# Optimization experiments

Measured on AMD Instinct MI355X. Metric: run time of the kernel, lower is better.

The kernel has to match this reference:

```python
import jax, jax.numpy as jnp
import numpy as np

_W = jnp.array([10., 9., 8., 7., 6., 5., 4., 3., 2., 1.], dtype=jnp.float32)
_W_NORM = _W / jnp.sum(_W)  # np.average normalizes by weight sum (55)


def setup_inputs() -> dict:
    key = jax.random.key(0)
    k1, k2 = jax.random.split(key)
    x = jax.random.randint(k1, (1024, 64, 10), 0, 8000, dtype=jnp.int32)
    table = jax.random.normal(k2, (8000, 256), dtype=jnp.float32)
    return {"x": x, "table": table}


def reference(x, table):
    # Gather per-char vectors: [T, F, 10, D]
    vecs = table[x]
    # Weighted average over the 10 chars (weights [10..1], normalized)
    return jnp.einsum('tfcd,c->tfd', vecs, _W_NORM)
```

## Files before the change

### kernel.cpp

```cpp
#include <hip/hip_runtime.h>
#include <hip/hip_bf16.h>


#define ROWS_TOTAL (1024 * 64)

typedef float v4f __attribute__((ext_vector_type(4)));

__global__ __launch_bounds__(256)
void char2vec_sliced2(const int* __restrict__ x,
                      const float* __restrict__ table,
                      float* __restrict__ out) {
    const int slice = blockIdx.x & 7;
    const int rgrp  = blockIdx.x >> 3;
    const int wave  = threadIdx.x >> 6;
    const int lane  = threadIdx.x & 63;

    const int row0 = rgrp * 64 + wave * 16 + (lane >> 3) * 2;
    const int row1 = row0 + 1;
    const int d    = slice * 32 + (lane & 7) * 4;

    const int2* __restrict__ xa = reinterpret_cast<const int2*>(x + row0 * 10);
    const int2* __restrict__ xb = reinterpret_cast<const int2*>(x + row1 * 10);
    int2 pa[5], pb[5];
#pragma unroll
    for (int i = 0; i < 5; ++i) pa[i] = xa[i];
#pragma unroll
    for (int i = 0; i < 5; ++i) pb[i] = xb[i];

    int ia[10], ib[10];
#pragma unroll
    for (int i = 0; i < 5; ++i) {
        ia[2 * i] = pa[i].x; ia[2 * i + 1] = pa[i].y;
        ib[2 * i] = pb[i].x; ib[2 * i + 1] = pb[i].y;
    }

    v4f va[10], vb[10];
#pragma unroll
    for (int c = 0; c < 10; ++c)
        va[c] = *reinterpret_cast<const v4f*>(table + (size_t)ia[c] * 256 + d);
#pragma unroll
    for (int c = 0; c < 10; ++c)
        vb[c] = *reinterpret_cast<const v4f*>(table + (size_t)ib[c] * 256 + d);

    const float w[10] = {10.f / 55.f, 9.f / 55.f, 8.f / 55.f, 7.f / 55.f,
                         6.f / 55.f,  5.f / 55.f, 4.f / 55.f, 3.f / 55.f,
                         2.f / 55.f,  1.f / 55.f};

    v4f acc0 = (v4f)0.0f, acc1 = (v4f)0.0f;
#pragma unroll
    for (int c = 0; c < 10; ++c) {
        acc0 += va[c] * w[c];
        acc1 += vb[c] * w[c];
    }

    __builtin_nontemporal_store(
        acc0, reinterpret_cast<v4f*>(out + (size_t)row0 * 256 + d));
    __builtin_nontemporal_store(
        acc1, reinterpret_cast<v4f*>(out + (size_t)row1 * 256 + d));
}

extern "C" void kernel_launch(void* const* d_in, const int* in_sizes, int n_in,
                              void* d_out, int out_size, void* d_ws, size_t ws_size,
                              hipStream_t stream) {
    const int*   x     = (const int*)d_in[0];
    const float* table = (const float*)d_in[1];
    float*       out   = (float*)d_out;

    const int blocks = (ROWS_TOTAL / 64) * 8;
    char2vec_sliced2<<<blocks, 256, 0, stream>>>(x, table, out);
}
```

Baseline: 31.95 us.

## Gather from fp16 copy of embedding table with wider per-thread tiles

Adds a pre-pass kernel that converts the fp32 table to fp16 in workspace on every call. The main kernel then gathers 16-byte fp16 vectors of 8 elements and accumulates in fp32, and each block now covers 128 rows. The aim is to halve gather traffic and raise bytes per load, at the cost of an extra conversion launch, a full pass over the table, and fp16 rounding error on the table values.

```diff
diff --git a/kernel.cpp b/kernel.cpp
--- a/kernel.cpp
+++ b/kernel.cpp
@@ -1,10 +1,85 @@
 #include <hip/hip_runtime.h>
-#include <hip/hip_bf16.h>
+#include <hip/hip_fp16.h>
 
 
-#define ROWS_TOTAL (1024 * 64)
+#define ROWS_TOTAL  (1024 * 64)
+#define TABLE_ROWS  8000
+#define TABLE_D     256
 
 typedef float v4f __attribute__((ext_vector_type(4)));
+typedef _Float16 h8 __attribute__((ext_vector_type(8)));
+
+__global__ __launch_bounds__(256)
+void cvt_table_f16(const float* __restrict__ t, _Float16* __restrict__ o) {
+    const size_t i = (size_t)blockIdx.x * 256 + threadIdx.x;
+    v4f v = *reinterpret_cast<const v4f*>(t + i * 4);
+    _Float16 r[4];
+    r[0] = (_Float16)v.x; r[1] = (_Float16)v.y;
+    r[2] = (_Float16)v.z; r[3] = (_Float16)v.w;
+    *reinterpret_cast<ushort4*>(o + i * 4) = *reinterpret_cast<ushort4*>(r);
+}
+
+__global__ __launch_bounds__(256)
+void char2vec_f16w(const int* __restrict__ x,
+                   const _Float16* __restrict__ tb,
+                   float* __restrict__ out) {
+    const int slice = blockIdx.x & 7;
+    const int rgrp  = blockIdx.x >> 3;
+    const int wave  = threadIdx.x >> 6;
+    const int lane  = threadIdx.x & 63;
+    const int g     = lane >> 2;
+    const int li    = lane & 3;
+
+    const int row0 = rgrp * 128 + wave * 32 + g * 2;
+    const int row1 = row0 + 1;
+    const int d    = slice * 32 + li * 8;
+
+    const int4* __restrict__ xi = reinterpret_cast<const int4*>(x + row0 * 10);
+    int4 q0 = xi[0], q1 = xi[1], q2 = xi[2], q3 = xi[3], q4 = xi[4];
+
+    int ia[10], ib[10];
+    ia[0] = q0.x; ia[1] = q0.y; ia[2] = q0.z; ia[3] = q0.w;
+    ia[4] = q1.x; ia[5] = q1.y; ia[6] = q1.z; ia[7] = q1.w;
+    ia[8] = q2.x; ia[9] = q2.y;
+    ib[0] = q2.z; ib[1] = q2.w;
+    ib[2] = q3.x; ib[3] = q3.y; ib[4] = q3.z; ib[5] = q3.w;
+    ib[6] = q4.x; ib[7] = q4.y; ib[8] = q4.z; ib[9] = q4.w;
+
+    h8 va[10], vb[10];
+#pragma unroll
+    for (int c = 0; c < 10; ++c)
+        va[c] = *reinterpret_cast<const h8*>(tb + (size_t)ia[c] * TABLE_D + d);
+#pragma unroll
+    for (int c = 0; c < 10; ++c)
+        vb[c] = *reinterpret_cast<const h8*>(tb + (size_t)ib[c] * TABLE_D + d);
+
+    const float w[10] = {10.f / 55.f, 9.f / 55.f, 8.f / 55.f, 7.f / 55.f,
+                         6.f / 55.f,  5.f / 55.f, 4.f / 55.f, 3.f / 55.f,
+                         2.f / 55.f,  1.f / 55.f};
+
+    float a0[8] = {0, 0, 0, 0, 0, 0, 0, 0};
+    float a1[8] = {0, 0, 0, 0, 0, 0, 0, 0};
+#pragma unroll
+    for (int c = 0; c < 10; ++c) {
+#pragma unroll
+        for (int e = 0; e < 8; ++e) {
+            a0[e] = fmaf((float)va[c][e], w[c], a0[e]);
+            a1[e] = fmaf((float)vb[c][e], w[c], a1[e]);
+        }
+    }
+
+    v4f s0lo = {a0[0], a0[1], a0[2], a0[3]};
+    v4f s0hi = {a0[4], a0[5], a0[6], a0[7]};
+    v4f s1lo = {a1[0], a1[1], a1[2], a1[3]};
+    v4f s1hi = {a1[4], a1[5], a1[6], a1[7]};
+
+    float* o0 = out + (size_t)row0 * 256 + d;
+    float* o1 = out + (size_t)row1 * 256 + d;
+    __builtin_nontemporal_store(s0lo, reinterpret_cast<v4f*>(o0));
+    __builtin_nontemporal_store(s0hi, reinterpret_cast<v4f*>(o0 + 4));
+    __builtin_nontemporal_store(s1lo, reinterpret_cast<v4f*>(o1));
+    __builtin_nontemporal_store(s1hi, reinterpret_cast<v4f*>(o1 + 4));
+}
 
 __global__ __launch_bounds__(256)
 void char2vec_sliced2(const int* __restrict__ x,
@@ -37,10 +112,10 @@
     v4f va[10], vb[10];
 #pragma unroll
     for (int c = 0; c < 10; ++c)
-        va[c] = *reinterpret_cast<const v4f*>(table + (size_t)ia[c] * 256 + d);
+        va[c] = *reinterpret_cast<const v4f*>(table + (size_t)ia[c] * TABLE_D + d);
 #pragma unroll
     for (int c = 0; c < 10; ++c)
-        vb[c] = *reinterpret_cast<const v4f*>(table + (size_t)ib[c] * 256 + d);
+        vb[c] = *reinterpret_cast<const v4f*>(table + (size_t)ib[c] * TABLE_D + d);
 
     const float w[10] = {10.f / 55.f, 9.f / 55.f, 8.f / 55.f, 7.f / 55.f,
                          6.f / 55.f,  5.f / 55.f, 4.f / 55.f, 3.f / 55.f,
@@ -66,6 +141,16 @@
     const float* table = (const float*)d_in[1];
     float*       out   = (float*)d_out;
 
-    const int blocks = (ROWS_TOTAL / 64) * 8;
-    char2vec_sliced2<<<blocks, 256, 0, stream>>>(x, table, out);
+    const size_t f16_bytes = (size_t)TABLE_ROWS * TABLE_D * sizeof(_Float16);
+
+    if (ws_size >= f16_bytes) {
+        _Float16* tb = (_Float16*)d_ws;
+        const int cvt_blocks = (TABLE_ROWS * TABLE_D / 4) / 256;
+        cvt_table_f16<<<cvt_blocks, 256, 0, stream>>>(table, tb);
+        const int blocks = (ROWS_TOTAL / 128) * 8;
+        char2vec_f16w<<<blocks, 256, 0, stream>>>(x, tb, out);
+    } else {
+        const int blocks = (ROWS_TOTAL / 64) * 8;
+        char2vec_sliced2<<<blocks, 256, 0, stream>>>(x, table, out);
+    }
 }
```

After: 40.32 us. 26.2% more time.

## Convert embedding table to fp16 in workspace and gather half-precision rows

Applied to the files above, without the earlier changes.

Adds a pre-pass that converts the fp32 table to fp16 in the workspace buffer, then gathers fp16 rows with one wave per output row and accumulates in fp32. The aim is to halve the bytes read by the random gathers, at the cost of an extra launch that reads 8 MB and writes 4 MB each call. Rounding the table to fp16 loses precision, which may exceed tolerance. The original fp32 kernel remains as a fallback when the workspace is too small.

```diff
diff --git a/kernel.cpp b/kernel.cpp
--- a/kernel.cpp
+++ b/kernel.cpp
@@ -1,10 +1,59 @@
 #include <hip/hip_runtime.h>
-#include <hip/hip_bf16.h>
+#include <hip/hip_fp16.h>
 
 
-#define ROWS_TOTAL (1024 * 64)
+#define ROWS_TOTAL  (1024 * 64)
+#define TABLE_ROWS  8000
+#define TABLE_D     256
 
 typedef float v4f __attribute__((ext_vector_type(4)));
+typedef _Float16 h4 __attribute__((ext_vector_type(4)));
+
+__global__ __launch_bounds__(256)
+void cvt_table_f16(const float* __restrict__ t, _Float16* __restrict__ o) {
+    const size_t i = (size_t)blockIdx.x * 256 + threadIdx.x;
+    v4f v = *reinterpret_cast<const v4f*>(t + i * 4);
+    _Float16 r[4];
+    r[0] = (_Float16)v.x; r[1] = (_Float16)v.y;
+    r[2] = (_Float16)v.z; r[3] = (_Float16)v.w;
+    *reinterpret_cast<ushort4*>(o + i * 4) = *reinterpret_cast<ushort4*>(r);
+}
+
+__global__ __launch_bounds__(256)
+void char2vec_row(const int* __restrict__ x,
+                  const _Float16* __restrict__ tb,
+                  float* __restrict__ out) {
+    const int wave = threadIdx.x >> 6;
+    const int lane = threadIdx.x & 63;
+    const int row  = blockIdx.x * 4 + wave;
+    const int d    = lane * 4;
+
+    const int2* __restrict__ xi = reinterpret_cast<const int2*>(x + row * 10);
+    int2 p0 = xi[0], p1 = xi[1], p2 = xi[2], p3 = xi[3], p4 = xi[4];
+    int idx[10] = {p0.x, p0.y, p1.x, p1.y, p2.x,
+                   p2.y, p3.x, p3.y, p4.x, p4.y};
+
+    h4 v[10];
+#pragma unroll
+    for (int c = 0; c < 10; ++c)
+        v[c] = *reinterpret_cast<const h4*>(tb + (size_t)idx[c] * TABLE_D + d);
+
+    const float w[10] = {10.f / 55.f, 9.f / 55.f, 8.f / 55.f, 7.f / 55.f,
+                         6.f / 55.f,  5.f / 55.f, 4.f / 55.f, 3.f / 55.f,
+                         2.f / 55.f,  1.f / 55.f};
+
+    v4f acc = (v4f)0.0f;
+#pragma unroll
+    for (int c = 0; c < 10; ++c) {
+        acc.x = fmaf((float)v[c][0], w[c], acc.x);
+        acc.y = fmaf((float)v[c][1], w[c], acc.y);
+        acc.z = fmaf((float)v[c][2], w[c], acc.z);
+        acc.w = fmaf((float)v[c][3], w[c], acc.w);
+    }
+
+    __builtin_nontemporal_store(
+        acc, reinterpret_cast<v4f*>(out + (size_t)row * 256 + d));
+}
 
 __global__ __launch_bounds__(256)
 void char2vec_sliced2(const int* __restrict__ x,
@@ -37,10 +86,10 @@
     v4f va[10], vb[10];
 #pragma unroll
     for (int c = 0; c < 10; ++c)
-        va[c] = *reinterpret_cast<const v4f*>(table + (size_t)ia[c] * 256 + d);
+        va[c] = *reinterpret_cast<const v4f*>(table + (size_t)ia[c] * TABLE_D + d);
 #pragma unroll
     for (int c = 0; c < 10; ++c)
-        vb[c] = *reinterpret_cast<const v4f*>(table + (size_t)ib[c] * 256 + d);
+        vb[c] = *reinterpret_cast<const v4f*>(table + (size_t)ib[c] * TABLE_D + d);
 
     const float w[10] = {10.f / 55.f, 9.f / 55.f, 8.f / 55.f, 7.f / 55.f,
                          6.f / 55.f,  5.f / 55.f, 4.f / 55.f, 3.f / 55.f,
@@ -66,6 +115,16 @@
     const float* table = (const float*)d_in[1];
     float*       out   = (float*)d_out;
 
-    const int blocks = (ROWS_TOTAL / 64) * 8;
-    char2vec_sliced2<<<blocks, 256, 0, stream>>>(x, table, out);
+    const size_t f16_bytes = (size_t)TABLE_ROWS * TABLE_D * sizeof(_Float16);
+
+    if (ws_size >= f16_bytes) {
+        _Float16* tb = (_Float16*)d_ws;
+        const int cvt_blocks = (TABLE_ROWS * TABLE_D / 4) / 256;
+        cvt_table_f16<<<cvt_blocks, 256, 0, stream>>>(table, tb);
+        const int blocks = ROWS_TOTAL / 4;
+        char2vec_row<<<blocks, 256, 0, stream>>>(x, tb, out);
+    } else {
+        const int blocks = (ROWS_TOTAL / 64) * 8;
+        char2vec_sliced2<<<blocks, 256, 0, stream>>>(x, table, out);
+    }
 }
```

After: 40.00 us. 25.2% more time.

## Convert table to permuted fp16 in workspace and gather half-width rows

Applied to the files above, without the earlier changes.

Adds a pre-pass kernel that converts the fp32 embedding table to fp16 in the workspace, permuted so each lane reads eight halves covering two four-float output chunks. The main kernel then gathers 16-byte fp16 vectors, accumulates in fp32, and has each wave handle two full rows, with indices loaded once and shared via shuffles. This halves the gather bytes but adds a full-table conversion launch on every call and loses precision relative to fp32 inputs.

```diff
diff --git a/kernel.cpp b/kernel.cpp
--- a/kernel.cpp
+++ b/kernel.cpp
@@ -1,10 +1,70 @@
 #include <hip/hip_runtime.h>
-#include <hip/hip_bf16.h>
+#include <hip/hip_fp16.h>
 
 
 #define ROWS_TOTAL (1024 * 64)
+#define TROWS 8000
+#define TD 256
 
 typedef float v4f __attribute__((ext_vector_type(4)));
+typedef _Float16 h8 __attribute__((ext_vector_type(8)));
+
+__global__ __launch_bounds__(256)
+void cvt_perm(const float* __restrict__ t, _Float16* __restrict__ o) {
+    const int tid = blockIdx.x * 256 + threadIdx.x;
+    const int row = tid >> 5;
+    const int m   = tid & 31;
+    const float* src = t + (size_t)row * TD + 4 * m;
+    v4f a = *reinterpret_cast<const v4f*>(src);
+    v4f b = *reinterpret_cast<const v4f*>(src + 128);
+    h8 r;
+    r[0] = (_Float16)a.x; r[1] = (_Float16)a.y;
+    r[2] = (_Float16)a.z; r[3] = (_Float16)a.w;
+    r[4] = (_Float16)b.x; r[5] = (_Float16)b.y;
+    r[6] = (_Float16)b.z; r[7] = (_Float16)b.w;
+    __builtin_nontemporal_store(r, reinterpret_cast<h8*>(o + (size_t)tid * 8));
+}
+
+__global__ __launch_bounds__(256)
+void char2vec_hw(const int* __restrict__ x,
+                 const _Float16* __restrict__ tb,
+                 float* __restrict__ out) {
+    const int l    = threadIdx.x & 63;
+    const int wave = threadIdx.x >> 6;
+    const int row0 = (blockIdx.x * 4 + wave) * 2;
+    const int half = l >> 5;
+    const int m    = l & 31;
+    const int row  = row0 + half;
+
+    const int t = x[row0 * 10 + (l < 20 ? l : 19)];
+
+    int idx[10];
+#pragma unroll
+    for (int c = 0; c < 10; ++c) idx[c] = __shfl(t, half * 10 + c);
+
+    h8 v[10];
+#pragma unroll
+    for (int c = 0; c < 10; ++c)
+        v[c] = *reinterpret_cast<const h8*>(tb + (size_t)idx[c] * TD + m * 8);
+
+    const float w[10] = {10.f / 55.f, 9.f / 55.f, 8.f / 55.f, 7.f / 55.f,
+                         6.f / 55.f,  5.f / 55.f, 4.f / 55.f, 3.f / 55.f,
+                         2.f / 55.f,  1.f / 55.f};
+
+    float acc[8] = {0, 0, 0, 0, 0, 0, 0, 0};
+#pragma unroll
+    for (int c = 0; c < 10; ++c) {
+#pragma unroll
+        for (int e = 0; e < 8; ++e)
+            acc[e] = fmaf((float)v[c][e], w[c], acc[e]);
+    }
+
+    v4f lo = {acc[0], acc[1], acc[2], acc[3]};
+    v4f hi = {acc[4], acc[5], acc[6], acc[7]};
+    float* orow = out + (size_t)row * TD;
+    __builtin_nontemporal_store(lo, reinterpret_cast<v4f*>(orow + 4 * m));
+    __builtin_nontemporal_store(hi, reinterpret_cast<v4f*>(orow + 128 + 4 * m));
+}
 
 __global__ __launch_bounds__(256)
 void char2vec_sliced2(const int* __restrict__ x,
@@ -37,10 +97,10 @@
     v4f va[10], vb[10];
 #pragma unroll
     for (int c = 0; c < 10; ++c)
-        va[c] = *reinterpret_cast<const v4f*>(table + (size_t)ia[c] * 256 + d);
+        va[c] = *reinterpret_cast<const v4f*>(table + (size_t)ia[c] * TD + d);
 #pragma unroll
     for (int c = 0; c < 10; ++c)
-        vb[c] = *reinterpret_cast<const v4f*>(table + (size_t)ib[c] * 256 + d);
+        vb[c] = *reinterpret_cast<const v4f*>(table + (size_t)ib[c] * TD + d);
 
     const float w[10] = {10.f / 55.f, 9.f / 55.f, 8.f / 55.f, 7.f / 55.f,
                          6.f / 55.f,  5.f / 55.f, 4.f / 55.f, 3.f / 55.f,
@@ -54,9 +114,9 @@
     }
 
     __builtin_nontemporal_store(
-        acc0, reinterpret_cast<v4f*>(out + (size_t)row0 * 256 + d));
+        acc0, reinterpret_cast<v4f*>(out + (size_t)row0 * TD + d));
     __builtin_nontemporal_store(
-        acc1, reinterpret_cast<v4f*>(out + (size_t)row1 * 256 + d));
+        acc1, reinterpret_cast<v4f*>(out + (size_t)row1 * TD + d));
 }
 
 extern "C" void kernel_launch(void* const* d_in, const int* in_sizes, int n_in,
@@ -66,6 +126,14 @@
     const float* table = (const float*)d_in[1];
     float*       out   = (float*)d_out;
 
-    const int blocks = (ROWS_TOTAL / 64) * 8;
-    char2vec_sliced2<<<blocks, 256, 0, stream>>>(x, table, out);
+    const size_t f16_bytes = (size_t)TROWS * TD * sizeof(_Float16);
+
+    if (ws_size >= f16_bytes) {
+        _Float16* tb = (_Float16*)d_ws;
+        cvt_perm<<<(TROWS * 32) / 256, 256, 0, stream>>>(table, tb);
+        char2vec_hw<<<ROWS_TOTAL / 8, 256, 0, stream>>>(x, tb, out);
+    } else {
+        const int blocks = (ROWS_TOTAL / 64) * 8;
+        char2vec_sliced2<<<blocks, 256, 0, stream>>>(x, table, out);
+    }
 }
```

Measured after the change: 31.60 us. No clear change (-1.1%).
